# Kernel tuning notes

Measured on AMD Instinct MI355X. Metric: run time of the kernel, lower is better.

The kernel has to match this reference:

```python
import jax, jax.numpy as jnp
import numpy as np

S = 100                     # MC weight samples
B = 128                     # batch
CONV1 = (100, 20, 1, 5, 5)  # (S, Cout, Cin, kh, kw)
CONV2 = (100, 50, 20, 5, 5)
AFF1 = (100, 500, 800)      # (S, out, in)
AFF2 = (100, 10, 500)
W_OFF = np.cumsum([0, 500, 25000, 400000, 5000])
B_OFF = np.cumsum([0, 20, 50, 500, 10])
NW, NB = 430500, 580


def _softplus(r):
    return jnp.log1p(jnp.exp(r))  # sigma_T(rho) = log(1 + exp(rho))


def _conv(h, w, b):
    # h: (B, S or 1, Cin, H, W); w: (S, Cout, Cin, kh, kw); b: (S, Cout)
    def one(xs, ws):  # xs: (B,Cin,H,W), ws: (Cout,Cin,kh,kw)
        return jax.lax.conv_general_dilated(xs, ws, (1, 1), 'VALID')
    if h.shape[1] == 1:  # shared input broadcast over samples (first layer)
        out = jax.vmap(one, in_axes=(None, 0), out_axes=1)(h[:, 0], w)
    else:
        out = jax.vmap(one, in_axes=(1, 0), out_axes=1)(h, w)
    return out + b[None, :, :, None, None]  # (B,S,Cout,H',W')


def _maxpool(h):  # 2x2 stride-2 over trailing spatial dims
    return jax.lax.reduce_window(h, -jnp.inf, jax.lax.max,
                                 (1, 1, 1, 2, 2), (1, 1, 1, 2, 2), 'VALID')


def setup_inputs() -> dict:
    key = jax.random.key(0)
    ks = jax.random.split(key, 4)
    x = jax.random.normal(ks[0], (B, 1, 28, 28), dtype=jnp.float32)
    e = jax.random.normal(ks[1], (S, NW + NB), dtype=jnp.float32)
    mu_w = jax.random.normal(ks[2], (NW,), dtype=jnp.float32) * 0.05
    rho_w = jnp.ones((NW,), dtype=jnp.float32) * 0.5
    mu_b = jax.random.normal(ks[3], (NB,), dtype=jnp.float32) * 0.05
    rho_b = jnp.ones((NB,), dtype=jnp.float32) * 0.5
    return {"x": x, "e": e, "mu_w": mu_w, "rho_w": rho_w,
            "mu_b": mu_b, "rho_b": rho_b}


def reference(x, e, mu_w, rho_w, mu_b, rho_b):
    # reparameterized per-sample weights: (S, NW) and (S, NB)
    w = mu_w + _softplus(rho_w) * e[:, :NW]
    b = mu_b + _softplus(rho_b) * e[:, NW:]

    h = x[:, None]  # (B,1,1,28,28): singleton MC dim broadcasts
    # conv1 + relu + pool
    h = _conv(h, w[:, W_OFF[0]:W_OFF[1]].reshape(CONV1), b[:, B_OFF[0]:B_OFF[1]])
    h = _maxpool(jax.nn.relu(h))                     # (B,S,20,12,12)
    # conv2 + relu + pool
    h = _conv(h, w[:, W_OFF[1]:W_OFF[2]].reshape(CONV2), b[:, B_OFF[1]:B_OFF[2]])
    h = _maxpool(jax.nn.relu(h))                     # (B,S,50,4,4)
    h = h.reshape(h.shape[0], h.shape[1], -1)        # (B,S,800)
    # aff1 + relu
    w3 = w[:, W_OFF[2]:W_OFF[3]].reshape(AFF1)
    h = jax.nn.relu(jnp.einsum('bsi,soi->bso', h, w3) + b[None, :, B_OFF[2]:B_OFF[3]])
    # aff2 + log_softmax
    w4 = w[:, W_OFF[3]:W_OFF[4]].reshape(AFF2)
    h = jnp.einsum('bsi,soi->bso', h, w4) + b[None, :, B_OFF[3]:B_OFF[4]]
    h = jax.nn.log_softmax(h, axis=-1)               # (B,S,10)
    return h.mean(axis=1)                            # eval path: mean over MC samples
```

## Files before the change

### kernel.cpp

```cpp
#include <hip/hip_runtime.h>
#include <math.h>

#define Sn 100
#define Bn 128
#define NWc 430500
#define EWc 431080

typedef __attribute__((ext_vector_type(8)))  short bhalf8;
typedef __attribute__((ext_vector_type(16))) float fx16;

__device__ __forceinline__ float sp_f(float r){
    return fmaxf(r, 0.f) + log1pf(__expf(-fabsf(r)));
}
__device__ __forceinline__ ushort bfr(float f){
    union { float f; uint u; } c; c.f = f;
    uint r = (c.u + 0x7FFFu + ((c.u >> 16) & 1u)) >> 16;
    return (ushort)r;
}

__global__ void k00_sp(const float* __restrict__ rho_w, const float* __restrict__ rho_b,
                       float* __restrict__ sp_all){
    int i = blockIdx.x * blockDim.x + threadIdx.x;
    if (i < NWc)      sp_all[i] = sp_f(rho_w[i]);
    else if (i < EWc) sp_all[i] = sp_f(rho_b[i - NWc]);
}

__global__ __launch_bounds__(256) void k0_w3t(const float* __restrict__ e,
        const float* __restrict__ mu_w, const float* __restrict__ sp_all,
        ushort* __restrict__ w3){
    __shared__ __align__(16) ushort ls[2][20*808];
    int oc = blockIdx.x;
    int sp = blockIdx.y;
    int s0 = sp * 2;
    int o0 = oc * 20;
    int tid = threadIdx.x;
    const float* e0 = e + (size_t)s0*EWc + 25500 + (size_t)o0*800;
    const float* e1 = e0 + EWc;
    const float* mb = mu_w   + 25500 + (size_t)o0*800;
    const float* pb = sp_all + 25500 + (size_t)o0*800;
    #pragma unroll 2
    for (int j = tid; j < 4000; j += 256){
        int o = j / 200, k4 = j - o*200;
        float4 mv = *(const float4*)(mb + j*4);
        float4 sv = *(const float4*)(pb + j*4);
        float4 ev0 = *(const float4*)(e0 + j*4);
        float4 ev1 = *(const float4*)(e1 + j*4);
        ushort4 t0, t1;
        t0.x = bfr(fmaf(sv.x, ev0.x, mv.x));
        t0.y = bfr(fmaf(sv.y, ev0.y, mv.y));
        t0.z = bfr(fmaf(sv.z, ev0.z, mv.z));
        t0.w = bfr(fmaf(sv.w, ev0.w, mv.w));
        t1.x = bfr(fmaf(sv.x, ev1.x, mv.x));
        t1.y = bfr(fmaf(sv.y, ev1.y, mv.y));
        t1.z = bfr(fmaf(sv.z, ev1.z, mv.z));
        t1.w = bfr(fmaf(sv.w, ev1.w, mv.w));
        *(ushort4*)&ls[0][o*808 + k4*4] = t0;
        *(ushort4*)&ls[1][o*808 + k4*4] = t1;
    }
    __syncthreads();
    if (tid < 200){
        int kt = tid >> 3, l8 = tid & 7;
        #pragma unroll
        for (int ss = 0; ss < 2; ++ss){
            ushort* wb = w3 + (size_t)(s0 + ss)*400000 + kt*16000 + o0*32;
            #pragma unroll
            for (int it = 0; it < 10; ++it){
                int idx = it*8 + l8;
                int o = idx >> 2, kp = (idx & 3)*8;
                uint4 v = *(const uint4*)&ls[ss][o*808 + kt*32 + kp];
                *(uint4*)(wb + idx*8) = v;
            }
        }
    }
}

__global__ void k0_small(const float* __restrict__ e, const float* __restrict__ mu_w,
                       const float* __restrict__ sp_all, const float* __restrict__ mu_b,
                       float* __restrict__ w1, ushort* __restrict__ w2r,
                       float* __restrict__ w4, float* __restrict__ ball){
    const int per = 31080;
    int idx = blockIdx.x * blockDim.x + threadIdx.x;
    if (idx >= Sn * per) return;
    int s = idx / per, j = idx % per;
    if (j < 500){
        float v = fmaf(sp_all[j], e[(size_t)s*EWc + j], mu_w[j]);
        w1[s*500 + j] = v;
    } else if (j < 25500){
        int g = j;
        float v = fmaf(sp_all[g], e[(size_t)s*EWc + g], mu_w[g]);
        int j2 = j - 500;
        int oc = j2 / 500, rem = j2 % 500;
        int ic = rem / 25, kk = rem % 25;
        w2r[(size_t)s*51200 + (kk*64 + oc)*32 + ic] = bfr(v);
    } else if (j < 30500){
        int g = 425500 + (j - 25500);
        float v = fmaf(sp_all[g], e[(size_t)s*EWc + g], mu_w[g]);
        w4[s*5000 + (j - 25500)] = v;
    } else {
        int k = j - 30500;
        float v = fmaf(sp_all[NWc + k], e[(size_t)s*EWc + NWc + k], mu_b[k]);
        ball[s*580 + k] = v;
    }
}

__global__ __launch_bounds__(256, 2) void k1_conv1(const float* __restrict__ x,
        const float* __restrict__ w1, const float* __restrict__ ball,
        ushort* __restrict__ h1p){
    __shared__ __align__(16) float xs[784];
    __shared__ __align__(16) float w1s[500];
    __shared__ float b1s[20];
    __shared__ __align__(16) ushort ots[2880];
    int bid = blockIdx.x;
    int s = bid / Bn, b = bid % Bn;
    int tid = threadIdx.x;
    for (int i = tid; i < 784; i += 256) xs[i] = x[b*784 + i];
    for (int i = tid; i < 500; i += 256) w1s[i] = w1[s*500 + i];
    if (tid < 20) b1s[tid] = ball[s*580 + tid];
    __syncthreads();
    if (tid < 240){
        int c = tid / 12, y = tid % 12;

        float acc0[24], acc1[24];
        #pragma unroll
        for (int i = 0; i < 24; ++i){ acc0[i] = 0.f; acc1[i] = 0.f; }

        #pragma unroll
        for (int ky = 0; ky < 5; ++ky){
            float rlo[28], rhi[28];
            const float* plo = &xs[(2*y + ky) * 28];
            const float* phi = &xs[(2*y + ky + 1) * 28];
            #pragma unroll
            for (int cc = 0; cc < 28; cc += 4){
                float4 v0 = *(const float4*)(plo + cc);
                rlo[cc] = v0.x; rlo[cc+1] = v0.y; rlo[cc+2] = v0.z; rlo[cc+3] = v0.w;
                float4 v1 = *(const float4*)(phi + cc);
                rhi[cc] = v1.x; rhi[cc+1] = v1.y; rhi[cc+2] = v1.z; rhi[cc+3] = v1.w;
            }
            #pragma unroll
            for (int kx = 0; kx < 5; ++kx){
                float wv = w1s[c*25 + ky*5 + kx];
                #pragma unroll
                for (int cx = 0; cx < 24; ++cx){
                    acc0[cx] = fmaf(rlo[cx + kx], wv, acc0[cx]);
                    acc1[cx] = fmaf(rhi[cx + kx], wv, acc1[cx]);
                }
            }
        }
        float bias = b1s[c];
        #pragma unroll
        for (int px = 0; px < 12; ++px){
            float m = fmaxf(fmaxf(acc0[2*px], acc0[2*px+1]),
                            fmaxf(acc1[2*px], acc1[2*px+1]));
            ots[(y*12 + px)*20 + c] = bfr(fmaxf(m + bias, 0.f));
        }
    }
    __syncthreads();
    const uint* o32 = (const uint*)ots;
    uint* g32 = (uint*)(h1p + (s*Bn + b)*2880);
    for (int j = tid; j < 1440; j += 256) g32[j] = o32[j];
}

__global__ __launch_bounds__(256, 4) void k2_direct(const ushort* __restrict__ h1p,
        const ushort* __restrict__ w2r, const float* __restrict__ ball,
        ushort* __restrict__ h2p){
    __shared__ __align__(16) ushort img[4*3456];
    __shared__ __align__(16) ushort Bls[2][2048];
    int bid = blockIdx.x;
    int s = bid >> 5, g = bid & 31;
    int tid = threadIdx.x;
    const uint* g32 = (const uint*)(h1p + (size_t)(s*Bn + g*4)*2880);
    uint* l32 = (uint*)img;
    for (int j = tid; j < 5760; j += 256){
        int im = j / 1440, r = j - im*1440;
        int p = r / 10, u = r - p*10;
        l32[im*1728 + p*12 + u] = g32[j];
    }
    for (int j = tid; j < 1152; j += 256){
        int im = j / 288, r = j - im*288;
        int p = r >> 1, u = 10 + (r & 1);
        l32[im*1728 + p*12 + u] = 0u;
    }

    int oc_w = tid >> 2, c_w = tid & 3;
    int P = ((c_w >> 1)*2 + (oc_w >> 5))*64 + (c_w & 1)*32 + (oc_w & 31);
    uint4* bd0 = (uint4*)&Bls[0][P*8];
    uint4* bd1 = (uint4*)&Bls[1][P*8];
    const uint4* bsrc = (const uint4*)(w2r + (size_t)(s*25)*2048) + tid;
    uint4 breg = bsrc[0];
    *bd0 = breg;

    int wv = tid >> 6, l = tid & 63;
    int l31 = l & 31, q = l >> 5;
    const ushort* imgw = img + wv*3456;
    int pixb0 = ((l31      ) >> 3)*12 + (l31 & 7);
    int pixb1 = ((l31 + 32 ) >> 3)*12 + (l31 & 7);
    int lam = q*32 + l31;
    fx16 acc00 = (fx16)0.f, acc01 = (fx16)0.f, acc10 = (fx16)0.f, acc11 = (fx16)0.f;
    const bhalf8 zero8 = (bhalf8)(short)0;

    __syncthreads();

    #pragma unroll 1
    for (int kk = 0; kk < 25; ++kk){
        int cur = kk & 1;
        if (kk < 24) breg = bsrc[(kk + 1)*256];

        int ky = kk / 5, kx = kk - ky*5;
        int poff = ky*12 + kx;
        const ushort* r0 = imgw + (pixb0 + poff)*24;
        const ushort* r1 = imgw + (pixb1 + poff)*24;
        const ushort* Bc = Bls[cur];

        bhalf8 a00 = *(const bhalf8*)(r0 + q*8);
        bhalf8 a10 = *(const bhalf8*)(r1 + q*8);
        bhalf8 b0  = *(const bhalf8*)&Bc[       lam*8];
        bhalf8 b1  = *(const bhalf8*)&Bc[ 512 + lam*8];
        acc00 = __builtin_amdgcn_mfma_f32_32x32x16_bf16(a00, b0, acc00, 0, 0, 0);
        acc01 = __builtin_amdgcn_mfma_f32_32x32x16_bf16(a00, b1, acc01, 0, 0, 0);
        acc10 = __builtin_amdgcn_mfma_f32_32x32x16_bf16(a10, b0, acc10, 0, 0, 0);
        acc11 = __builtin_amdgcn_mfma_f32_32x32x16_bf16(a10, b1, acc11, 0, 0, 0);

        bhalf8 a01 = (q == 0) ? *(const bhalf8*)(r0 + 16) : zero8;
        bhalf8 a11 = (q == 0) ? *(const bhalf8*)(r1 + 16) : zero8;
        bhalf8 b2  = *(const bhalf8*)&Bc[1024 + lam*8];
        bhalf8 b3  = *(const bhalf8*)&Bc[1536 + lam*8];
        acc00 = __builtin_amdgcn_mfma_f32_32x32x16_bf16(a01, b2, acc00, 0, 0, 0);
        acc01 = __builtin_amdgcn_mfma_f32_32x32x16_bf16(a01, b3, acc01, 0, 0, 0);
        acc10 = __builtin_amdgcn_mfma_f32_32x32x16_bf16(a11, b2, acc10, 0, 0, 0);
        acc11 = __builtin_amdgcn_mfma_f32_32x32x16_bf16(a11, b3, acc11, 0, 0, 0);

        if (kk < 24){
            *(cur ? bd0 : bd1) = breg;
            __syncthreads();
        }
    }
    int b = g*4 + wv;
    ushort* dst = h2p + (size_t)s*102400 + (size_t)b*32;
    #pragma unroll
    for (int nt = 0; nt < 2; ++nt){
        int oc = nt*32 + l31;
        if (oc >= 50) continue;
        float bias = ball[s*580 + 20 + oc];
        #pragma unroll
        for (int mt = 0; mt < 2; ++mt){
            fx16 a;
            if (nt == 0) a = mt ? acc10 : acc00;
            else         a = mt ? acc11 : acc01;
            #pragma unroll
            for (int gp = 0; gp < 2; ++gp){
                float p0 = fmaxf(fmaxf(a[8*gp+0], a[8*gp+1]), fmaxf(a[8*gp+4], a[8*gp+5]));
                float p1 = fmaxf(fmaxf(a[8*gp+2], a[8*gp+3]), fmaxf(a[8*gp+6], a[8*gp+7]));
                p0 = fmaxf(p0 + bias, 0.f);
                p1 = fmaxf(p1 + bias, 0.f);
                int py = mt*2 + gp;
                int i  = oc*16 + py*4 + 2*q;
                uint pk = (uint)bfr(p0) | ((uint)bfr(p1) << 16);
                *(uint*)(dst + (i >> 5)*4096 + (i & 31)) = pk;
            }
        }
    }
}

#define ICS 40
__global__ __launch_bounds__(256) void k3_mfma(const ushort* __restrict__ h2p,
        const ushort* __restrict__ w3, const float* __restrict__ ball,
        float* __restrict__ h3){
    __shared__ __align__(16) ushort As[128*ICS];
    __shared__ __align__(16) ushort Bsh[64*ICS];
    int bid = blockIdx.x;
    int s = bid >> 3, nblk = bid & 7;
    int o0 = nblk * 64;
    int tid = threadIdx.x;
    int wv = tid >> 6, l = tid & 63, l31 = l & 31, q = l >> 5;
    int wm = wv >> 1, wn = wv & 1;
    fx16 acc0 = (fx16)0.f, acc1 = (fx16)0.f;
    int rr = tid >> 2, rk = (tid & 3)*8;
    const ushort* Abase = h2p + (size_t)s*102400;
    const ushort* Bbase = w3  + (size_t)s*400000 + (size_t)o0*32;
    bool bvalid = (o0 + rr) < 500;
    const uint4 z4 = make_uint4(0u,0u,0u,0u);

    uint4 ar0, ar1, br;
    ar0 = *(const uint4*)(Abase + rr*32 + rk);
    ar1 = *(const uint4*)(Abase + (rr + 64)*32 + rk);
    br  = bvalid ? *(const uint4*)(Bbase + rr*32 + rk) : z4;

    for (int kt = 0; kt < 25; ++kt){
        __syncthreads();
        *(uint4*)&As[rr*ICS + rk]        = ar0;
        *(uint4*)&As[(rr + 64)*ICS + rk] = ar1;
        *(uint4*)&Bsh[rr*ICS + rk]       = br;
        __syncthreads();
        if (kt < 24){
            ar0 = *(const uint4*)(Abase + (kt+1)*4096 + rr*32 + rk);
            ar1 = *(const uint4*)(Abase + (kt+1)*4096 + (rr + 64)*32 + rk);
            br  = bvalid ? *(const uint4*)(Bbase + (kt+1)*16000 + rr*32 + rk) : z4;
        }
        #pragma unroll
        for (int ks = 0; ks < 2; ++ks){
            bhalf8 a0 = *(const bhalf8*)&As[(wm*64      + l31)*ICS + ks*16 + q*8];
            bhalf8 a1 = *(const bhalf8*)&As[(wm*64 + 32 + l31)*ICS + ks*16 + q*8];
            bhalf8 bb = *(const bhalf8*)&Bsh[(wn*32 + l31)*ICS + ks*16 + q*8];
            acc0 = __builtin_amdgcn_mfma_f32_32x32x16_bf16(a0, bb, acc0, 0, 0, 0);
            acc1 = __builtin_amdgcn_mfma_f32_32x32x16_bf16(a1, bb, acc1, 0, 0, 0);
        }
    }
    int o = o0 + wn*32 + l31;
    if (o < 500){
        float bias = ball[s*580 + 70 + o];
        #pragma unroll
        for (int mt = 0; mt < 2; ++mt){
            fx16 a = mt ? acc1 : acc0;
            #pragma unroll
            for (int reg = 0; reg < 16; ++reg){
                int row = (reg & 3) + 8*(reg >> 2) + 4*q;
                int b = wm*64 + mt*32 + row;
                h3[(size_t)(s*Bn + b)*500 + o] = fmaxf(a[reg] + bias, 0.f);
            }
        }
    }
}

__global__ __launch_bounds__(256) void k4a(const float* __restrict__ h3,
        const float* __restrict__ w4, const float* __restrict__ ball,
        float* __restrict__ lsw){
    int wv = threadIdx.x >> 6, lane = threadIdx.x & 63;
    int p = blockIdx.x*4 + wv;
    int s = p / Bn;
    const float* hp = &h3[(size_t)p*500];
    const float* wp = &w4[(size_t)s*5000];
    float part[10];
    #pragma unroll
    for (int o = 0; o < 10; ++o) part[o] = 0.f;
    for (int i = lane; i < 500; i += 64){
        float hv = hp[i];
        #pragma unroll
        for (int o = 0; o < 10; ++o)
            part[o] = fmaf(hv, wp[o*500 + i], part[o]);
    }
    #pragma unroll
    for (int o = 0; o < 10; ++o){
        #pragma unroll
        for (int d = 1; d < 64; d <<= 1)
            part[o] += __shfl_xor(part[o], d);
    }
    float v[10]; float m = -INFINITY;
    #pragma unroll
    for (int o = 0; o < 10; ++o){
        v[o] = part[o] + ball[s*580 + 570 + o];
        m = fmaxf(m, v[o]);
    }
    float sum = 0.f;
    #pragma unroll
    for (int o = 0; o < 10; ++o) sum += __expf(v[o] - m);
    float lse = m + __logf(sum);
    if (lane == 0){
        #pragma unroll
        for (int o = 0; o < 10; ++o) lsw[p*10 + o] = v[o] - lse;
    }
}

__global__ void k4b(const float* __restrict__ lsw, float* __restrict__ outp){
    int j = blockIdx.x * blockDim.x + threadIdx.x;
    if (j >= Bn*10) return;
    int b = j / 10, o = j % 10;
    float acc = 0.f;
    for (int s2 = 0; s2 < Sn; ++s2) acc += lsw[(s2*Bn + b)*10 + o];
    outp[j] = acc * (1.f / (float)Sn);
}

extern "C" void kernel_launch(void* const* d_in, const int* in_sizes, int n_in,
                              void* d_out, int out_size, void* d_ws, size_t ws_size,
                              hipStream_t stream){
    const float* x     = (const float*)d_in[0];
    const float* e     = (const float*)d_in[1];
    const float* mu_w  = (const float*)d_in[2];
    const float* rho_w = (const float*)d_in[3];
    const float* mu_b  = (const float*)d_in[4];
    const float* rho_b = (const float*)d_in[5];
    float* ws   = (float*)d_ws;
    float* w1     = ws;
    float* w4     = w1 + 50000;
    float* ball   = w4 + 500000;
    float* h3     = ball + 58000;
    float* lsw    = h3 + 6400000;
    float* sp_all = lsw + 128000;
    ushort* h1p = (ushort*)(sp_all + 431080);
    ushort* h2p = h1p + 36864000;
    ushort* w2r = h2p + 10240000;
    ushort* w3  = w2r + 5120000;
    float* outp = (float*)d_out;

    hipMemsetAsync(w2r, 0, (size_t)Sn*51200*2, stream);
    k00_sp   <<<(EWc + 255)/256, 256, 0, stream>>>(rho_w, rho_b, sp_all);
    k0_w3t   <<<dim3(25, 50), 256, 0, stream>>>(e, mu_w, sp_all, w3);
    k0_small <<<(Sn*31080 + 255)/256, 256, 0, stream>>>(e, mu_w, sp_all, mu_b, w1, w2r, w4, ball);
    k1_conv1 <<<Sn*Bn, 256, 0, stream>>>(x, w1, ball, h1p);
    k2_direct<<<Sn*32, 256, 0, stream>>>(h1p, w2r, ball, h2p);
    k3_mfma  <<<Sn*8, 256, 0, stream>>>(h2p, w3, ball, h3);
    k4a      <<<3200, 256, 0, stream>>>(h3, w4, ball, lsw);
    k4b      <<<(Bn*10 + 255)/256, 256, 0, stream>>>(lsw, outp);
}
```

Baseline: 525.8 us.

## Fuse aff1 weight reparameterization into the MFMA GEMM B-tile load

```diff
diff --git a/kernel.cpp b/kernel.cpp
--- a/kernel.cpp
+++ b/kernel.cpp
@@ -23,55 +23,6 @@
     int i = blockIdx.x * blockDim.x + threadIdx.x;
     if (i < NWc)      sp_all[i] = sp_f(rho_w[i]);
     else if (i < EWc) sp_all[i] = sp_f(rho_b[i - NWc]);
-}
-
-__global__ __launch_bounds__(256) void k0_w3t(const float* __restrict__ e,
-        const float* __restrict__ mu_w, const float* __restrict__ sp_all,
-        ushort* __restrict__ w3){
-    __shared__ __align__(16) ushort ls[2][20*808];
-    int oc = blockIdx.x;
-    int sp = blockIdx.y;
-    int s0 = sp * 2;
-    int o0 = oc * 20;
-    int tid = threadIdx.x;
-    const float* e0 = e + (size_t)s0*EWc + 25500 + (size_t)o0*800;
-    const float* e1 = e0 + EWc;
-    const float* mb = mu_w   + 25500 + (size_t)o0*800;
-    const float* pb = sp_all + 25500 + (size_t)o0*800;
-    #pragma unroll 2
-    for (int j = tid; j < 4000; j += 256){
-        int o = j / 200, k4 = j - o*200;
-        float4 mv = *(const float4*)(mb + j*4);
-        float4 sv = *(const float4*)(pb + j*4);
-        float4 ev0 = *(const float4*)(e0 + j*4);
-        float4 ev1 = *(const float4*)(e1 + j*4);
-        ushort4 t0, t1;
-        t0.x = bfr(fmaf(sv.x, ev0.x, mv.x));
-        t0.y = bfr(fmaf(sv.y, ev0.y, mv.y));
-        t0.z = bfr(fmaf(sv.z, ev0.z, mv.z));
-        t0.w = bfr(fmaf(sv.w, ev0.w, mv.w));
-        t1.x = bfr(fmaf(sv.x, ev1.x, mv.x));
-        t1.y = bfr(fmaf(sv.y, ev1.y, mv.y));
-        t1.z = bfr(fmaf(sv.z, ev1.z, mv.z));
-        t1.w = bfr(fmaf(sv.w, ev1.w, mv.w));
-        *(ushort4*)&ls[0][o*808 + k4*4] = t0;
-        *(ushort4*)&ls[1][o*808 + k4*4] = t1;
-    }
-    __syncthreads();
-    if (tid < 200){
-        int kt = tid >> 3, l8 = tid & 7;
-        #pragma unroll
-        for (int ss = 0; ss < 2; ++ss){
-            ushort* wb = w3 + (size_t)(s0 + ss)*400000 + kt*16000 + o0*32;
-            #pragma unroll
-            for (int it = 0; it < 10; ++it){
-                int idx = it*8 + l8;
-                int o = idx >> 2, kp = (idx & 3)*8;
-                uint4 v = *(const uint4*)&ls[ss][o*808 + kt*32 + kp];
-                *(uint4*)(wb + idx*8) = v;
-            }
-        }
-    }
 }
 
 __global__ void k0_small(const float* __restrict__ e, const float* __restrict__ mu_w,
@@ -263,7 +214,8 @@
 
 #define ICS 40
 __global__ __launch_bounds__(256) void k3_mfma(const ushort* __restrict__ h2p,
-        const ushort* __restrict__ w3, const float* __restrict__ ball,
+        const float* __restrict__ e, const float* __restrict__ mu_w,
+        const float* __restrict__ sp_all, const float* __restrict__ ball,
         float* __restrict__ h3){
     __shared__ __align__(16) ushort As[128*ICS];
     __shared__ __align__(16) ushort Bsh[64*ICS];
@@ -276,25 +228,48 @@
     fx16 acc0 = (fx16)0.f, acc1 = (fx16)0.f;
     int rr = tid >> 2, rk = (tid & 3)*8;
     const ushort* Abase = h2p + (size_t)s*102400;
-    const ushort* Bbase = w3  + (size_t)s*400000 + (size_t)o0*32;
+    size_t gb = 25500 + (size_t)(o0 + rr)*800 + rk;
+    const float* eb = e + (size_t)s*EWc + gb;
+    const float* mb = mu_w   + gb;
+    const float* pb = sp_all + gb;
     bool bvalid = (o0 + rr) < 500;
-    const uint4 z4 = make_uint4(0u,0u,0u,0u);
-
-    uint4 ar0, ar1, br;
+
+    uint4 ar0, ar1;
+    float4 ev0, ev1, mv0, mv1, pv0, pv1;
     ar0 = *(const uint4*)(Abase + rr*32 + rk);
     ar1 = *(const uint4*)(Abase + (rr + 64)*32 + rk);
-    br  = bvalid ? *(const uint4*)(Bbase + rr*32 + rk) : z4;
+    if (bvalid){
+        ev0 = *(const float4*)(eb);     ev1 = *(const float4*)(eb + 4);
+        mv0 = *(const float4*)(mb);     mv1 = *(const float4*)(mb + 4);
+        pv0 = *(const float4*)(pb);     pv1 = *(const float4*)(pb + 4);
+    }
 
     for (int kt = 0; kt < 25; ++kt){
         __syncthreads();
         *(uint4*)&As[rr*ICS + rk]        = ar0;
         *(uint4*)&As[(rr + 64)*ICS + rk] = ar1;
-        *(uint4*)&Bsh[rr*ICS + rk]       = br;
+        uint4 brv = make_uint4(0u,0u,0u,0u);
+        if (bvalid){
+            brv.x = (uint)bfr(fmaf(pv0.x, ev0.x, mv0.x)) |
+                    ((uint)bfr(fmaf(pv0.y, ev0.y, mv0.y)) << 16);
+            brv.y = (uint)bfr(fmaf(pv0.z, ev0.z, mv0.z)) |
+                    ((uint)bfr(fmaf(pv0.w, ev0.w, mv0.w)) << 16);
+            brv.z = (uint)bfr(fmaf(pv1.x, ev1.x, mv1.x)) |
+                    ((uint)bfr(fmaf(pv1.y, ev1.y, mv1.y)) << 16);
+            brv.w = (uint)bfr(fmaf(pv1.z, ev1.z, mv1.z)) |
+                    ((uint)bfr(fmaf(pv1.w, ev1.w, mv1.w)) << 16);
+        }
+        *(uint4*)&Bsh[rr*ICS + rk] = brv;
         __syncthreads();
         if (kt < 24){
+            int ko = (kt + 1)*32;
             ar0 = *(const uint4*)(Abase + (kt+1)*4096 + rr*32 + rk);
             ar1 = *(const uint4*)(Abase + (kt+1)*4096 + (rr + 64)*32 + rk);
-            br  = bvalid ? *(const uint4*)(Bbase + (kt+1)*16000 + rr*32 + rk) : z4;
+            if (bvalid){
+                ev0 = *(const float4*)(eb + ko);     ev1 = *(const float4*)(eb + ko + 4);
+                mv0 = *(const float4*)(mb + ko);     mv1 = *(const float4*)(mb + ko + 4);
+                pv0 = *(const float4*)(pb + ko);     pv1 = *(const float4*)(pb + ko + 4);
+            }
         }
         #pragma unroll
         for (int ks = 0; ks < 2; ++ks){
@@ -388,16 +363,14 @@
     ushort* h1p = (ushort*)(sp_all + 431080);
     ushort* h2p = h1p + 36864000;
     ushort* w2r = h2p + 10240000;
-    ushort* w3  = w2r + 5120000;
     float* outp = (float*)d_out;
 
     hipMemsetAsync(w2r, 0, (size_t)Sn*51200*2, stream);
     k00_sp   <<<(EWc + 255)/256, 256, 0, stream>>>(rho_w, rho_b, sp_all);
-    k0_w3t   <<<dim3(25, 50), 256, 0, stream>>>(e, mu_w, sp_all, w3);
     k0_small <<<(Sn*31080 + 255)/256, 256, 0, stream>>>(e, mu_w, sp_all, mu_b, w1, w2r, w4, ball);
     k1_conv1 <<<Sn*Bn, 256, 0, stream>>>(x, w1, ball, h1p);
     k2_direct<<<Sn*32, 256, 0, stream>>>(h1p, w2r, ball, h2p);
-    k3_mfma  <<<Sn*8, 256, 0, stream>>>(h2p, w3, ball, h3);
+    k3_mfma  <<<Sn*8, 256, 0, stream>>>(h2p, e, mu_w, sp_all, ball, h3);
     k4a      <<<3200, 256, 0, stream>>>(h3, w4, ball, lsw);
     k4b      <<<(Bn*10 + 255)/256, 256, 0, stream>>>(lsw, outp);
 }
```

After: 544.9 us. +3.6%, slower.

## Rewrite conv1 as im2col bf16 MFMA GEMM with fused pool

Applied to the files above, without the earlier changes.

```diff
diff --git a/kernel.cpp b/kernel.cpp
--- a/kernel.cpp
+++ b/kernel.cpp
@@ -103,55 +103,79 @@
     }
 }
 
-__global__ __launch_bounds__(256, 2) void k1_conv1(const float* __restrict__ x,
+__global__ __launch_bounds__(256, 3) void k1_conv1(const float* __restrict__ x,
         const float* __restrict__ w1, const float* __restrict__ ball,
         ushort* __restrict__ h1p){
     __shared__ __align__(16) float xs[784];
-    __shared__ __align__(16) float w1s[500];
-    __shared__ float b1s[20];
+    __shared__ __align__(16) ushort As[576*32];
+    __shared__ __align__(16) ushort w1b[1024];
     __shared__ __align__(16) ushort ots[2880];
     int bid = blockIdx.x;
     int s = bid / Bn, b = bid % Bn;
     int tid = threadIdx.x;
     for (int i = tid; i < 784; i += 256) xs[i] = x[b*784 + i];
-    for (int i = tid; i < 500; i += 256) w1s[i] = w1[s*500 + i];
-    if (tid < 20) b1s[tid] = ball[s*580 + tid];
+    {
+        int i0 = tid*4;
+        int oc = i0 >> 5, k0 = i0 & 31;
+        ushort4 v; ushort* vp = (ushort*)&v;
+        #pragma unroll
+        for (int jj = 0; jj < 4; ++jj){
+            int k = k0 + jj;
+            vp[jj] = (oc < 20 && k < 25) ? bfr(w1[s*500 + oc*25 + k]) : (ushort)0;
+        }
+        *(ushort4*)&w1b[i0] = v;
+    }
     __syncthreads();
-    if (tid < 240){
-        int c = tid / 12, y = tid % 12;
-
-        float acc0[24], acc1[24];
-        #pragma unroll
-        for (int i = 0; i < 24; ++i){ acc0[i] = 0.f; acc1[i] = 0.f; }
-
+
+    for (int p = tid; p < 576; p += 256){
+        int quad = p >> 2, sub = p & 3;
+        int yp = quad / 12, xp = quad - yp*12;
+        int y = 2*yp + (sub >> 1), xx = 2*xp + (sub & 1);
+        ushort vals[25];
         #pragma unroll
         for (int ky = 0; ky < 5; ++ky){
-            float rlo[28], rhi[28];
-            const float* plo = &xs[(2*y + ky) * 28];
-            const float* phi = &xs[(2*y + ky + 1) * 28];
+            const float* rowp = &xs[(y + ky)*28 + xx];
             #pragma unroll
-            for (int cc = 0; cc < 28; cc += 4){
-                float4 v0 = *(const float4*)(plo + cc);
-                rlo[cc] = v0.x; rlo[cc+1] = v0.y; rlo[cc+2] = v0.z; rlo[cc+3] = v0.w;
-                float4 v1 = *(const float4*)(phi + cc);
-                rhi[cc] = v1.x; rhi[cc+1] = v1.y; rhi[cc+2] = v1.z; rhi[cc+3] = v1.w;
+            for (int kx = 0; kx < 5; ++kx)
+                vals[ky*5 + kx] = bfr(rowp[kx]);
+        }
+        uint pk[16];
+        #pragma unroll
+        for (int j = 0; j < 12; ++j)
+            pk[j] = (uint)vals[2*j] | ((uint)vals[2*j+1] << 16);
+        pk[12] = (uint)vals[24];
+        pk[13] = 0u; pk[14] = 0u; pk[15] = 0u;
+        uint* dst = (uint*)As;
+        int base = p*16, sw = (p & 7) << 2;
+        #pragma unroll
+        for (int c = 0; c < 4; ++c)
+            *(uint4*)&dst[(base + c*4) ^ sw] =
+                make_uint4(pk[c*4], pk[c*4+1], pk[c*4+2], pk[c*4+3]);
+    }
+
+    int wv = tid >> 6, l = tid & 63;
+    int l31 = l & 31, q = l >> 5;
+    __syncthreads();
+    bhalf8 b0 = *(const bhalf8*)&w1b[l31*32 +      q*8];
+    bhalf8 b1 = *(const bhalf8*)&w1b[l31*32 + 16 + q*8];
+    float bias = (l31 < 20) ? ball[s*580 + l31] : 0.f;
+
+    for (int t = wv; t < 18; t += 4){
+        int row0 = t*32 + l31;
+        int swz = (row0 & 7) << 3;
+        bhalf8 a0 = *(const bhalf8*)&As[(row0*32 +      q*8) ^ swz];
+        bhalf8 a1 = *(const bhalf8*)&As[(row0*32 + 16 + q*8) ^ swz];
+        fx16 acc = (fx16)0.f;
+        acc = __builtin_amdgcn_mfma_f32_32x32x16_bf16(a0, b0, acc, 0, 0, 0);
+        acc = __builtin_amdgcn_mfma_f32_32x32x16_bf16(a1, b1, acc, 0, 0, 0);
+        if (l31 < 20){
+            #pragma unroll
+            for (int rg = 0; rg < 4; ++rg){
+                float m = fmaxf(fmaxf(acc[4*rg], acc[4*rg+1]),
+                                fmaxf(acc[4*rg+2], acc[4*rg+3]));
+                int pout = t*8 + 2*rg + q;
+                ots[pout*20 + l31] = bfr(fmaxf(m + bias, 0.f));
             }
-            #pragma unroll
-            for (int kx = 0; kx < 5; ++kx){
-                float wv = w1s[c*25 + ky*5 + kx];
-                #pragma unroll
-                for (int cx = 0; cx < 24; ++cx){
-                    acc0[cx] = fmaf(rlo[cx + kx], wv, acc0[cx]);
-                    acc1[cx] = fmaf(rhi[cx + kx], wv, acc1[cx]);
-                }
-            }
-        }
-        float bias = b1s[c];
-        #pragma unroll
-        for (int px = 0; px < 12; ++px){
-            float m = fmaxf(fmaxf(acc0[2*px], acc0[2*px+1]),
-                            fmaxf(acc1[2*px], acc1[2*px+1]));
-            ots[(y*12 + px)*20 + c] = bfr(fmaxf(m + bias, 0.f));
         }
     }
     __syncthreads();
```

After: 517.4 us. Within noise of the previous version (-1.6%).
